# Kernel optimization log

Hardware: AMD Instinct MI355X
Metric: run time of the kernel (lower is better)

## Reference

```python
import jax, jax.numpy as jnp
import numpy as np

EPS_NORM = 1e-12  # F.normalize eps
EPS_BN = 1e-5     # BatchNorm1d eps


def _gather_neighbors(tensor, index):
    # tensor: (bs, v, d), index: (bs, v, n) -> (bs, v, n, d)
    return jax.vmap(lambda t, i: t[i])(tensor, index)


def setup_inputs() -> dict:
    key = jax.random.key(0)
    ks = jax.random.split(key, 8)
    bs, v, n = 4, 4096, 32
    cin, cout = 128, 256
    stdv = float(np.sqrt(2.0 / cout))
    return {
        "neighbor_index": jax.random.randint(ks[0], (bs, v, n), 0, v),
        "vertices": jax.random.normal(ks[1], (bs, v, 3), dtype=jnp.float32),
        "feature_map": jax.random.normal(ks[2], (bs, v, cin - 1), dtype=jnp.float32),
        "directions": jax.random.uniform(ks[3], (4, cout), minval=-stdv, maxval=stdv, dtype=jnp.float32),
        "W": jax.random.normal(ks[4], (cout, cin), dtype=jnp.float32) / np.sqrt(cin),
        "b": jnp.zeros((cout,), jnp.float32),
        "gamma": jnp.ones((cout,), jnp.float32),
        "beta": jnp.zeros((cout,), jnp.float32),
    }


def reference(neighbor_index, vertices, feature_map, directions, W, b, gamma, beta):
    # --- direction-based weights theta: (bs, v, n, cout) ---
    neighbors = _gather_neighbors(vertices, neighbor_index)          # (bs,v,n,3)
    direc = neighbors - vertices[:, :, None, :]
    direc_norm = direc / jnp.maximum(
        jnp.linalg.norm(direc, axis=-1, keepdims=True), EPS_NORM)    # F.normalize
    dir_w = (direc_norm + 1.0) * 0.5                                  # (bs,v,n,3)
    sup_w = jnp.stack([directions[1] - directions[0],
                       directions[2] - directions[0],
                       directions[3] - directions[0]], axis=0)        # (3, cout)
    theta = jax.nn.relu(jnp.einsum('bvnk,kc->bvnc', dir_w, sup_w) + directions[0])

    # --- gathered features + L2 distance channel ---
    fs = _gather_neighbors(feature_map, neighbor_index)               # (bs,v,n,cin-1)
    fdist = jnp.sqrt(jnp.sum(fs * fs, axis=-1, keepdims=True))        # (bs,v,n,1)
    fs = jnp.concatenate([fs, fdist], axis=-1)                        # (bs,v,n,cin)

    # --- Linear -> BatchNorm1d (training stats) -> ReLU ---
    z = jnp.einsum('bvni,ci->bvnc', fs, W) + b                        # (bs,v,n,cout)
    mean = jnp.mean(z, axis=(0, 1, 2))
    var = jnp.mean(jnp.square(z - mean), axis=(0, 1, 2))              # biased var
    zn = (z - mean) * jax.lax.rsqrt(var + EPS_BN) * gamma + beta
    act = jax.nn.relu(zn) * theta

    # --- max-pool over neighbor dim ---
    return jnp.max(act, axis=2)                                       # (bs,v,cout)
```

## Files before the change

kernel.cpp:

```cpp
#include <hip/hip_runtime.h>

typedef unsigned short ushort_t;
typedef __attribute__((ext_vector_type(8))) short short8;
typedef __attribute__((ext_vector_type(4))) float floatx4;
typedef __attribute__((ext_vector_type(2))) float floatx2;

#define NN    32
#define CIN   128
#define COUT  256
#define NPTS  16384
#define NSAMP (NPTS * NN)
#define LDA   136

__device__ ushort_t g_fsp[(size_t)NPTS * 128];
__device__ ushort_t g_wb[COUT * CIN];
__device__ ushort_t g_y[(size_t)NPTS * COUT];
__device__ int      g_mult[NPTS];
__device__ float    g_stat[512];
__device__ float    g_consts[1536];
__device__ int      g_isf32;

__device__ __forceinline__ float bf2f(ushort_t u) {
    return __uint_as_float(((unsigned int)u) << 16);
}
__device__ __forceinline__ ushort_t f2bf(float f) {
    unsigned int x = __float_as_uint(f);
    return (ushort_t)((x + 0x7FFFu + ((x >> 16) & 1u)) >> 16);
}

__global__ void detect_zero_kernel(const void* __restrict__ verts) {
    int tid = threadIdx.x;
    g_mult[blockIdx.x * 256 + tid] = 0;
    if (blockIdx.x == 0) {
        g_stat[tid] = 0.0f; g_stat[256 + tid] = 0.0f;
        if (tid < 64) {
            float ax = fabsf(bf2f(((const ushort_t*)verts)[tid]));
            bool plaus = (ax > 1e-5f) && (ax < 32.0f);
            unsigned long long b = __ballot(plaus);
            if (tid == 0) g_isf32 = (__popcll(b) >= 56) ? 0 : 1;
        }
    }
}

__global__ void prep_kernel(const void* __restrict__ fm,
                            const void* __restrict__ Wg,
                            const int* __restrict__ nbr) {
    const int f32 = g_isf32;
    const int tid = threadIdx.x;
    if (blockIdx.x < 32) {
        int i = blockIdx.x * 1024 + tid * 4;
        if (f32) {
            float4 v = ((const float4*)Wg)[i >> 2];
            g_wb[i] = f2bf(v.x); g_wb[i + 1] = f2bf(v.y);
            g_wb[i + 2] = f2bf(v.z); g_wb[i + 3] = f2bf(v.w);
        } else {
            *(uint2*)(g_wb + i) = *(const uint2*)((const ushort_t*)Wg + i);
        }
    }
    int gid = blockIdx.x * 256 + tid;
    if (gid < NSAMP) {
        int gv = ((gid >> 17) << 12) + nbr[gid];
        atomicAdd(&g_mult[gv], 1);
    }
    int row  = blockIdx.x * 4 + (tid >> 6);
    int lane = tid & 63;
    float f0, f1; ushort_t u0, u1;
    if (f32) {
        const float* src = (const float*)fm + (size_t)row * 127;
        f0 = src[lane];
        f1 = (lane < 63) ? src[64 + lane] : 0.0f;
        u0 = f2bf(f0); u1 = f2bf(f1);
    } else {
        const ushort_t* src = (const ushort_t*)fm + (size_t)row * 127;
        u0 = src[lane];
        u1 = (lane < 63) ? src[64 + lane] : (ushort_t)0;
        f0 = bf2f(u0); f1 = bf2f(u1);
    }
    float ss = f0 * f0 + f1 * f1;
    #pragma unroll
    for (int d = 1; d < 64; d <<= 1) ss += __shfl_xor(ss, d, 64);
    float fd = sqrtf(ss);
    ushort_t* dst = g_fsp + (size_t)row * 128;
    dst[lane]      = u0;
    dst[64 + lane] = (lane < 63) ? u1 : f2bf(fd);
}

__global__ __launch_bounds__(256, 2)
void ygemm_kernel() {
    __shared__ ushort_t At[64 * LDA];
    __shared__ float    multS[64];

    const int tid = threadIdx.x;
    const int r0  = blockIdx.x * 64;

    if (tid < 64) multS[tid] = (float)g_mult[r0 + tid];
    #pragma unroll
    for (int i = 0; i < 4; ++i) {
        int chunk = tid + i * 256;
        int r = chunk >> 4;
        int c = chunk & 15;
        const uint4 v = *(const uint4*)(g_fsp + (size_t)(r0 + r) * 128 + c * 8);
        *(uint4*)&At[r * LDA + c * 8] = v;
    }
    __syncthreads();

    const int lane = tid & 63;
    const int w    = tid >> 6;
    const int m    = lane & 15;
    const int q    = lane >> 4;

    floatx4 acc[4][4];
    #pragma unroll
    for (int rt = 0; rt < 4; ++rt)
        #pragma unroll
        for (int ct = 0; ct < 4; ++ct)
            acc[rt][ct] = (floatx4){0.0f, 0.0f, 0.0f, 0.0f};

    #pragma unroll
    for (int kk = 0; kk < 4; ++kk) {
        const int kof = kk * 32 + q * 8;
        short8 af[4];
        #pragma unroll
        for (int rt = 0; rt < 4; ++rt)
            af[rt] = *(const short8*)&At[(rt * 16 + m) * LDA + kof];
        short8 bfr[4];
        #pragma unroll
        for (int ct = 0; ct < 4; ++ct) {
            int ch = w * 64 + ct * 16 + m;
            bfr[ct] = *(const short8*)(g_wb + ch * CIN + kof);
        }
        #pragma unroll
        for (int rt = 0; rt < 4; ++rt)
            #pragma unroll
            for (int ct = 0; ct < 4; ++ct)
                acc[rt][ct] = __builtin_amdgcn_mfma_f32_16x16x32_bf16(
                    af[rt], bfr[ct], acc[rt][ct], 0, 0, 0);
    }

    #pragma unroll
    for (int ct = 0; ct < 4; ++ct) {
        const int ch = w * 64 + ct * 16 + m;
        float s = 0.0f, ss = 0.0f;
        #pragma unroll
        for (int rt = 0; rt < 4; ++rt)
            #pragma unroll
            for (int j = 0; j < 4; ++j) {
                int rloc = rt * 16 + q * 4 + j;
                ushort_t yb = f2bf(acc[rt][ct][j]);
                g_y[(size_t)(r0 + rloc) * COUT + ch] = yb;
                float yv = bf2f(yb);
                float wm = multS[rloc];
                s  += wm * yv;
                ss += wm * yv * yv;
            }
        s  += __shfl_xor(s, 16, 64);  s  += __shfl_xor(s, 32, 64);
        ss += __shfl_xor(ss, 16, 64); ss += __shfl_xor(ss, 32, 64);
        if (q == 0) {
            atomicAdd(&g_stat[ch], s);
            atomicAdd(&g_stat[256 + ch], ss);
        }
    }
}

__global__ void finalize_kernel(const void* __restrict__ gamma,
                                const void* __restrict__ beta,
                                const void* __restrict__ dirs) {
    const int f32 = g_isf32;
    int c = threadIdx.x;
    const float invN = 1.0f / (float)NSAMP;
    float mean = g_stat[c] * invN;
    float var  = fmaxf(g_stat[256 + c] * invN - mean * mean, 0.0f);
    float inv  = 1.0f / sqrtf(var + 1e-5f);
    float ga, be, d0, d1, d2, d3;
    if (f32) {
        ga = ((const float*)gamma)[c]; be = ((const float*)beta)[c];
        const float* dd = (const float*)dirs;
        d0 = dd[c]; d1 = dd[256 + c]; d2 = dd[512 + c]; d3 = dd[768 + c];
    } else {
        ga = bf2f(((const ushort_t*)gamma)[c]); be = bf2f(((const ushort_t*)beta)[c]);
        const ushort_t* dd = (const ushort_t*)dirs;
        d0 = bf2f(dd[c]); d1 = bf2f(dd[256 + c]);
        d2 = bf2f(dd[512 + c]); d3 = bf2f(dd[768 + c]);
    }
    float scale = ga * inv;
    g_consts[c]        = scale;
    g_consts[256 + c]  = be - mean * scale;
    g_consts[512 + c]  = d0;
    g_consts[768 + c]  = d1 - d0;
    g_consts[1024 + c] = d2 - d0;
    g_consts[1280 + c] = d3 - d0;
}

__global__ __launch_bounds__(128, 4)
void epi_kernel(const int* __restrict__ nbr,
                const void* __restrict__ verts,
                void* __restrict__ out) {
    __shared__ int    rows[NN];
    __shared__ float4 dws[NN];

    const int p   = blockIdx.x;
    const int tid = threadIdx.x;
    const int f32 = g_isf32;

    if (tid < NN) {
        int gv = ((p >> 12) << 12) + nbr[p * NN + tid];
        rows[tid] = gv;
        float sx, sy, sz, nx, ny, nz;
        if (f32) {
            const float* vv = (const float*)verts;
            sx = vv[p * 3]; sy = vv[p * 3 + 1]; sz = vv[p * 3 + 2];
            nx = vv[gv * 3]; ny = vv[gv * 3 + 1]; nz = vv[gv * 3 + 2];
        } else {
            const ushort_t* vv = (const ushort_t*)verts;
            sx = bf2f(vv[p * 3]); sy = bf2f(vv[p * 3 + 1]); sz = bf2f(vv[p * 3 + 2]);
            nx = bf2f(vv[gv * 3]); ny = bf2f(vv[gv * 3 + 1]); nz = bf2f(vv[gv * 3 + 2]);
        }
        float dx = nx - sx, dy = ny - sy, dz = nz - sz;
        float nrm = sqrtf(dx * dx + dy * dy + dz * dz);
        float inv = 1.0f / fmaxf(nrm, 1e-12f);
        dws[tid] = make_float4((dx * inv + 1.0f) * 0.5f,
                               (dy * inv + 1.0f) * 0.5f,
                               (dz * inv + 1.0f) * 0.5f, 0.0f);
    }
    __syncthreads();

    const int c2 = tid * 2;
    const floatx2 zero = {0.0f, 0.0f};
    floatx2 sc = *(const floatx2*)&g_consts[c2];
    floatx2 sh = *(const floatx2*)&g_consts[256 + c2];
    floatx2 d0 = *(const floatx2*)&g_consts[512 + c2];
    floatx2 s0 = *(const floatx2*)&g_consts[768 + c2];
    floatx2 s1 = *(const floatx2*)&g_consts[1024 + c2];
    floatx2 s2 = *(const floatx2*)&g_consts[1280 + c2];

    floatx2 vm0 = zero, vm1 = zero, vm2 = zero, vm3 = zero;
    #pragma unroll
    for (int j = 0; j < NN; j += 4) {
        #pragma unroll
        for (int jj = 0; jj < 4; ++jj) {
            int rb = __builtin_amdgcn_readfirstlane(rows[j + jj]);
            const unsigned int* rp =
                (const unsigned int*)(g_y + (size_t)rb * COUT);
            unsigned int u = rp[tid];
            floatx2 y;
            y.x = __uint_as_float(u << 16);
            y.y = __uint_as_float(u & 0xFFFF0000u);
            float4 dw = dws[j + jj];
            floatx2 th = d0 + s0 * dw.x + s1 * dw.y + s2 * dw.z;
            th = __builtin_elementwise_max(th, zero);
            floatx2 zt = (y * sc + sh) * th;
            if      (jj == 0) vm0 = __builtin_elementwise_max(vm0, zt);
            else if (jj == 1) vm1 = __builtin_elementwise_max(vm1, zt);
            else if (jj == 2) vm2 = __builtin_elementwise_max(vm2, zt);
            else              vm3 = __builtin_elementwise_max(vm3, zt);
        }
    }
    floatx2 vm = __builtin_elementwise_max(
        __builtin_elementwise_max(vm0, vm1),
        __builtin_elementwise_max(vm2, vm3));

    size_t ofs = (size_t)p * COUT + c2;
    if (f32) {
        *(floatx2*)((float*)out + ofs) = vm;
    } else {
        unsigned int o = ((unsigned int)f2bf(vm.y) << 16) | (unsigned int)f2bf(vm.x);
        *(unsigned int*)((ushort_t*)out + ofs) = o;
    }
}

extern "C" void kernel_launch(void* const* d_in, const int* in_sizes, int n_in,
                              void* d_out, int out_size, void* d_ws, size_t ws_size,
                              hipStream_t stream) {
    const int* nbr   = (const int*)d_in[0];
    const void* verts = d_in[1];
    const void* fm    = d_in[2];
    const void* dirs  = d_in[3];
    const void* Wg    = d_in[4];
    const void* gamma = d_in[6];
    const void* beta  = d_in[7];
    (void)d_ws; (void)ws_size; (void)in_sizes; (void)n_in; (void)out_size;

    detect_zero_kernel<<<dim3(64), dim3(256), 0, stream>>>(verts);
    prep_kernel<<<dim3(NPTS / 4), dim3(256), 0, stream>>>(fm, Wg, nbr);
    ygemm_kernel<<<dim3(NPTS / 64), dim3(256), 0, stream>>>();
    finalize_kernel<<<dim3(1), dim3(256), 0, stream>>>(gamma, beta, dirs);
    epi_kernel<<<dim3(NPTS), dim3(128), 0, stream>>>(nbr, verts, d_out);
}
```

Measured before the change: 155.8 us.

## Fuse feature prep and BN finalize into GEMM, drop dtype detection kernel

Removes the dtype-detection kernel and the separate finalize kernel, and stops staging bf16 features in a global buffer. The GEMM kernel now reads fp32 features directly, computes the L2 distance channel, and converts to bf16 in shared memory. The last block, chosen with an atomic counter, computes the BatchNorm constants and resets the statistics, multiplicity and counter state for the next call. This cuts launches and a global round trip, but it assumes fp32 inputs and relies on atomic last-block ordering and on zeroed state carrying across calls.

```diff
diff --git a/kernel.cpp b/kernel.cpp
--- a/kernel.cpp
+++ b/kernel.cpp
@@ -11,14 +11,14 @@
 #define NPTS  16384
 #define NSAMP (NPTS * NN)
 #define LDA   136
-
-__device__ ushort_t g_fsp[(size_t)NPTS * 128];
+#define YBLK  256
+
 __device__ ushort_t g_wb[COUT * CIN];
 __device__ ushort_t g_y[(size_t)NPTS * COUT];
 __device__ int      g_mult[NPTS];
 __device__ float    g_stat[512];
 __device__ float    g_consts[1536];
-__device__ int      g_isf32;
+__device__ int      g_done;
 
 __device__ __forceinline__ float bf2f(ushort_t u) {
     return __uint_as_float(((unsigned int)u) << 16);
@@ -28,86 +28,55 @@
     return (ushort_t)((x + 0x7FFFu + ((x >> 16) & 1u)) >> 16);
 }
 
-__global__ void detect_zero_kernel(const void* __restrict__ verts) {
-    int tid = threadIdx.x;
-    g_mult[blockIdx.x * 256 + tid] = 0;
-    if (blockIdx.x == 0) {
-        g_stat[tid] = 0.0f; g_stat[256 + tid] = 0.0f;
-        if (tid < 64) {
-            float ax = fabsf(bf2f(((const ushort_t*)verts)[tid]));
-            bool plaus = (ax > 1e-5f) && (ax < 32.0f);
-            unsigned long long b = __ballot(plaus);
-            if (tid == 0) g_isf32 = (__popcll(b) >= 56) ? 0 : 1;
-        }
-    }
-}
-
-__global__ void prep_kernel(const void* __restrict__ fm,
-                            const void* __restrict__ Wg,
+__global__ void hist_kernel(const float* __restrict__ Wg,
                             const int* __restrict__ nbr) {
-    const int f32 = g_isf32;
     const int tid = threadIdx.x;
     if (blockIdx.x < 32) {
         int i = blockIdx.x * 1024 + tid * 4;
-        if (f32) {
-            float4 v = ((const float4*)Wg)[i >> 2];
-            g_wb[i] = f2bf(v.x); g_wb[i + 1] = f2bf(v.y);
-            g_wb[i + 2] = f2bf(v.z); g_wb[i + 3] = f2bf(v.w);
-        } else {
-            *(uint2*)(g_wb + i) = *(const uint2*)((const ushort_t*)Wg + i);
-        }
+        float4 v = ((const float4*)Wg)[i >> 2];
+        g_wb[i] = f2bf(v.x); g_wb[i + 1] = f2bf(v.y);
+        g_wb[i + 2] = f2bf(v.z); g_wb[i + 3] = f2bf(v.w);
     }
     int gid = blockIdx.x * 256 + tid;
-    if (gid < NSAMP) {
-        int gv = ((gid >> 17) << 12) + nbr[gid];
-        atomicAdd(&g_mult[gv], 1);
-    }
-    int row  = blockIdx.x * 4 + (tid >> 6);
-    int lane = tid & 63;
-    float f0, f1; ushort_t u0, u1;
-    if (f32) {
-        const float* src = (const float*)fm + (size_t)row * 127;
-        f0 = src[lane];
-        f1 = (lane < 63) ? src[64 + lane] : 0.0f;
-        u0 = f2bf(f0); u1 = f2bf(f1);
-    } else {
-        const ushort_t* src = (const ushort_t*)fm + (size_t)row * 127;
-        u0 = src[lane];
-        u1 = (lane < 63) ? src[64 + lane] : (ushort_t)0;
-        f0 = bf2f(u0); f1 = bf2f(u1);
-    }
-    float ss = f0 * f0 + f1 * f1;
-    #pragma unroll
-    for (int d = 1; d < 64; d <<= 1) ss += __shfl_xor(ss, d, 64);
-    float fd = sqrtf(ss);
-    ushort_t* dst = g_fsp + (size_t)row * 128;
-    dst[lane]      = u0;
-    dst[64 + lane] = (lane < 63) ? u1 : f2bf(fd);
+    int gv  = ((gid >> 17) << 12) + nbr[gid];
+    atomicAdd(&g_mult[gv], 1);
 }
 
 __global__ __launch_bounds__(256, 2)
-void ygemm_kernel() {
+void ygemm_kernel(const float* __restrict__ fm,
+                  const float* __restrict__ gamma,
+                  const float* __restrict__ beta,
+                  const float* __restrict__ dirs) {
     __shared__ ushort_t At[64 * LDA];
     __shared__ float    multS[64];
-
-    const int tid = threadIdx.x;
-    const int r0  = blockIdx.x * 64;
+    __shared__ int      lastS;
+
+    const int tid  = threadIdx.x;
+    const int r0   = blockIdx.x * 64;
+    const int lane = tid & 63;
+    const int wv   = tid >> 6;
 
     if (tid < 64) multS[tid] = (float)g_mult[r0 + tid];
-    #pragma unroll
-    for (int i = 0; i < 4; ++i) {
-        int chunk = tid + i * 256;
-        int r = chunk >> 4;
-        int c = chunk & 15;
-        const uint4 v = *(const uint4*)(g_fsp + (size_t)(r0 + r) * 128 + c * 8);
-        *(uint4*)&At[r * LDA + c * 8] = v;
-    }
-    __syncthreads();
-
-    const int lane = tid & 63;
-    const int w    = tid >> 6;
-    const int m    = lane & 15;
-    const int q    = lane >> 4;
+
+    #pragma unroll
+    for (int i = 0; i < 16; ++i) {
+        int rloc = wv * 16 + i;
+        const float* src = fm + (size_t)(r0 + rloc) * 127;
+        float f0 = src[lane];
+        float f1 = (lane < 63) ? src[64 + lane] : 0.0f;
+        float ss = f0 * f0 + f1 * f1;
+        #pragma unroll
+        for (int d = 1; d < 64; d <<= 1) ss += __shfl_xor(ss, d, 64);
+        float fd = sqrtf(ss);
+        At[rloc * LDA + lane]      = f2bf(f0);
+        At[rloc * LDA + 64 + lane] = (lane < 63) ? f2bf(f1) : f2bf(fd);
+    }
+    __syncthreads();
+
+    if (tid < 64) g_mult[r0 + tid] = 0;
+
+    const int m = lane & 15;
+    const int q = lane >> 4;
 
     floatx4 acc[4][4];
     #pragma unroll
@@ -126,7 +95,7 @@
         short8 bfr[4];
         #pragma unroll
         for (int ct = 0; ct < 4; ++ct) {
-            int ch = w * 64 + ct * 16 + m;
+            int ch = wv * 64 + ct * 16 + m;
             bfr[ct] = *(const short8*)(g_wb + ch * CIN + kof);
         }
         #pragma unroll
@@ -139,7 +108,7 @@
 
     #pragma unroll
     for (int ct = 0; ct < 4; ++ct) {
-        const int ch = w * 64 + ct * 16 + m;
+        const int ch = wv * 64 + ct * 16 + m;
         float s = 0.0f, ss = 0.0f;
         #pragma unroll
         for (int rt = 0; rt < 4; ++rt)
@@ -160,62 +129,52 @@
             atomicAdd(&g_stat[256 + ch], ss);
         }
     }
-}
-
-__global__ void finalize_kernel(const void* __restrict__ gamma,
-                                const void* __restrict__ beta,
-                                const void* __restrict__ dirs) {
-    const int f32 = g_isf32;
-    int c = threadIdx.x;
-    const float invN = 1.0f / (float)NSAMP;
-    float mean = g_stat[c] * invN;
-    float var  = fmaxf(g_stat[256 + c] * invN - mean * mean, 0.0f);
-    float inv  = 1.0f / sqrtf(var + 1e-5f);
-    float ga, be, d0, d1, d2, d3;
-    if (f32) {
-        ga = ((const float*)gamma)[c]; be = ((const float*)beta)[c];
-        const float* dd = (const float*)dirs;
-        d0 = dd[c]; d1 = dd[256 + c]; d2 = dd[512 + c]; d3 = dd[768 + c];
-    } else {
-        ga = bf2f(((const ushort_t*)gamma)[c]); be = bf2f(((const ushort_t*)beta)[c]);
-        const ushort_t* dd = (const ushort_t*)dirs;
-        d0 = bf2f(dd[c]); d1 = bf2f(dd[256 + c]);
-        d2 = bf2f(dd[512 + c]); d3 = bf2f(dd[768 + c]);
-    }
-    float scale = ga * inv;
-    g_consts[c]        = scale;
-    g_consts[256 + c]  = be - mean * scale;
-    g_consts[512 + c]  = d0;
-    g_consts[768 + c]  = d1 - d0;
-    g_consts[1024 + c] = d2 - d0;
-    g_consts[1280 + c] = d3 - d0;
+
+    __syncthreads();
+    if (tid == 0) {
+        __threadfence();
+        int old = atomicAdd(&g_done, 1);
+        lastS = (old == YBLK - 1) ? 1 : 0;
+    }
+    __syncthreads();
+    if (lastS) {
+        __threadfence();
+        int c = tid;
+        float sum = atomicAdd(&g_stat[c], 0.0f);
+        float ssq = atomicAdd(&g_stat[256 + c], 0.0f);
+        const float invN = 1.0f / (float)NSAMP;
+        float mean = sum * invN;
+        float var  = fmaxf(ssq * invN - mean * mean, 0.0f);
+        float inv  = 1.0f / sqrtf(var + 1e-5f);
+        float scale = gamma[c] * inv;
+        g_consts[c]        = scale;
+        g_consts[256 + c]  = beta[c] - mean * scale;
+        float d0 = dirs[c];
+        g_consts[512 + c]  = d0;
+        g_consts[768 + c]  = dirs[256 + c] - d0;
+        g_consts[1024 + c] = dirs[512 + c] - d0;
+        g_consts[1280 + c] = dirs[768 + c] - d0;
+        g_stat[c] = 0.0f; g_stat[256 + c] = 0.0f;
+        if (tid == 0) g_done = 0;
+    }
 }
 
 __global__ __launch_bounds__(128, 4)
 void epi_kernel(const int* __restrict__ nbr,
-                const void* __restrict__ verts,
-                void* __restrict__ out) {
+                const float* __restrict__ verts,
+                float* __restrict__ out) {
     __shared__ int    rows[NN];
     __shared__ float4 dws[NN];
 
     const int p   = blockIdx.x;
     const int tid = threadIdx.x;
-    const int f32 = g_isf32;
 
     if (tid < NN) {
         int gv = ((p >> 12) << 12) + nbr[p * NN + tid];
         rows[tid] = gv;
-        float sx, sy, sz, nx, ny, nz;
-        if (f32) {
-            const float* vv = (const float*)verts;
-            sx = vv[p * 3]; sy = vv[p * 3 + 1]; sz = vv[p * 3 + 2];
-            nx = vv[gv * 3]; ny = vv[gv * 3 + 1]; nz = vv[gv * 3 + 2];
-        } else {
-            const ushort_t* vv = (const ushort_t*)verts;
-            sx = bf2f(vv[p * 3]); sy = bf2f(vv[p * 3 + 1]); sz = bf2f(vv[p * 3 + 2]);
-            nx = bf2f(vv[gv * 3]); ny = bf2f(vv[gv * 3 + 1]); nz = bf2f(vv[gv * 3 + 2]);
-        }
-        float dx = nx - sx, dy = ny - sy, dz = nz - sz;
+        float dx = verts[gv * 3 + 0] - verts[p * 3 + 0];
+        float dy = verts[gv * 3 + 1] - verts[p * 3 + 1];
+        float dz = verts[gv * 3 + 2] - verts[p * 3 + 2];
         float nrm = sqrtf(dx * dx + dy * dy + dz * dz);
         float inv = 1.0f / fmaxf(nrm, 1e-12f);
         dws[tid] = make_float4((dx * inv + 1.0f) * 0.5f,
@@ -259,30 +218,22 @@
         __builtin_elementwise_max(vm0, vm1),
         __builtin_elementwise_max(vm2, vm3));
 
-    size_t ofs = (size_t)p * COUT + c2;
-    if (f32) {
-        *(floatx2*)((float*)out + ofs) = vm;
-    } else {
-        unsigned int o = ((unsigned int)f2bf(vm.y) << 16) | (unsigned int)f2bf(vm.x);
-        *(unsigned int*)((ushort_t*)out + ofs) = o;
-    }
+    *(floatx2*)(out + (size_t)p * COUT + c2) = vm;
 }
 
 extern "C" void kernel_launch(void* const* d_in, const int* in_sizes, int n_in,
                               void* d_out, int out_size, void* d_ws, size_t ws_size,
                               hipStream_t stream) {
-    const int* nbr   = (const int*)d_in[0];
-    const void* verts = d_in[1];
-    const void* fm    = d_in[2];
-    const void* dirs  = d_in[3];
-    const void* Wg    = d_in[4];
-    const void* gamma = d_in[6];
-    const void* beta  = d_in[7];
+    const int*   nbr   = (const int*)d_in[0];
+    const float* verts = (const float*)d_in[1];
+    const float* fm    = (const float*)d_in[2];
+    const float* dirs  = (const float*)d_in[3];
+    const float* Wg    = (const float*)d_in[4];
+    const float* gamma = (const float*)d_in[6];
+    const float* beta  = (const float*)d_in[7];
     (void)d_ws; (void)ws_size; (void)in_sizes; (void)n_in; (void)out_size;
 
-    detect_zero_kernel<<<dim3(64), dim3(256), 0, stream>>>(verts);
-    prep_kernel<<<dim3(NPTS / 4), dim3(256), 0, stream>>>(fm, Wg, nbr);
-    ygemm_kernel<<<dim3(NPTS / 64), dim3(256), 0, stream>>>();
-    finalize_kernel<<<dim3(1), dim3(256), 0, stream>>>(gamma, beta, dirs);
-    epi_kernel<<<dim3(NPTS), dim3(128), 0, stream>>>(nbr, verts, d_out);
-}
+    hist_kernel<<<dim3(NSAMP / 256), dim3(256), 0, stream>>>(Wg, nbr);
+    ygemm_kernel<<<dim3(YBLK), dim3(256), 0, stream>>>(fm, gamma, beta, dirs);
+    epi_kernel<<<dim3(NPTS), dim3(128), 0, stream>>>(nbr, verts, (float*)d_out);
+}
```

Measured after the change: 170.0 us. 9.1% more time.
